# Kernel tuning notes

Hardware: AMD Instinct MI355X
Metric: run time of the kernel (lower is better)

Reference implementation:

```python
import jax, jax.numpy as jnp
import numpy as np

N = 8192            # n_nodes
E = 262144          # n_edges (avg degree 32)
IN_F, HID_F, OUT_F = 256, 128, 64


def _xavier(key, shape):
    fan_out, fan_in = shape
    lim = np.sqrt(6.0 / (fan_in + fan_out))
    return jax.random.uniform(key, shape, jnp.float32, -lim, lim)


def setup_inputs() -> dict:
    key = jax.random.key(0)
    k = jax.random.split(key, 7)
    edge_src = jnp.sort(jax.random.randint(k[0], (E,), 0, N))
    edge_dst = jax.random.randint(k[1], (E,), 0, N)
    h = jax.random.normal(k[2], (N, IN_F), jnp.float32)
    W0 = _xavier(k[3], (HID_F, IN_F))
    Wmu = _xavier(k[4], (OUT_F, HID_F))
    Wls = _xavier(k[5], (OUT_F, HID_F)) * 0.1  # keep exp(log_sigma) tame
    eps = jax.random.normal(k[6], (N, OUT_F), jnp.float32)
    return {"h": h, "W0": W0, "Wmu": Wmu, "Wls": Wls, "eps": eps,
            "edge_src": edge_src, "edge_dst": edge_dst}


def _gcn(edge_src, edge_dst, h, W, act=None):
    # a is the unweighted sparse adjacency given by (edge_src -> row, edge_dst -> col)
    n = h.shape[0]
    deg = jax.ops.segment_sum(jnp.ones(edge_src.shape[0], h.dtype), edge_src,
                              num_segments=n)                    # row-sum of a
    norm = jnp.clip(deg, 1.0, None) ** -0.5                      # d^{-1/2}, clamp(min=1)
    h = h * norm[:, None]                                        # pre-norm
    h = h @ W.T                                                  # Linear (no bias)
    h = jax.ops.segment_sum(h[edge_dst], edge_src, num_segments=n)  # a @ h (SpMM)
    h = h * norm[:, None]                                        # post-norm
    if act is not None:
        h = act(h)
    return h


def reference(h, W0, Wmu, Wls, eps, edge_src, edge_dst):
    h1 = _gcn(edge_src, edge_dst, h, W0, jax.nn.relu)            # gcn0 + ReLU
    mu = _gcn(edge_src, edge_dst, h1, Wmu)                       # gcn_mu
    log_sigma = _gcn(edge_src, edge_dst, h1, Wls)                # gcn_log_sigma
    z = mu + jnp.exp(log_sigma) * eps                            # q_z.rsample()
    logits = z @ z.T                                             # Bernoulli logits [N, N]
    return logits
```

## Files before the change

kernel.cpp:

```cpp
#include <hip/hip_runtime.h>
#include <hip/hip_bf16.h>
#include <cstdint>
#include <cstddef>

#define NN 8192
#define IN_F 256
#define HID_F 128
#define OUT_F 64

typedef __attribute__((ext_vector_type(8))) short short8v;
typedef __attribute__((ext_vector_type(4))) float f32x4;
typedef __attribute__((ext_vector_type(4))) unsigned short ushort4v;

static __device__ __forceinline__ unsigned short f2bf(float x) {
    unsigned int u = __float_as_uint(x);
    unsigned int r = (u + 0x7fffu + ((u >> 16) & 1u)) >> 16;
    return (unsigned short)r;
}
static __device__ __forceinline__ float bf2f(unsigned short u) {
    return __uint_as_float(((unsigned int)u) << 16);
}

__global__ void k_rowptr(const int* __restrict__ src, int* __restrict__ rp, int E, int N) {
    int i = blockIdx.x * blockDim.x + threadIdx.x;
    if (i >= E) return;
    int s = src[i];
    int p = (i == 0) ? -1 : src[i - 1];
    for (int n = p + 1; n <= s; ++n) rp[n] = i;
    if (i == E - 1) {
        for (int n = s + 1; n <= N; ++n) rp[n] = E;
    }
}

__global__ void k_norm(const int* __restrict__ rp, float* __restrict__ norm, int N) {
    int n = blockIdx.x * blockDim.x + threadIdx.x;
    if (n >= N) return;
    int d = rp[n + 1] - rp[n];
    float df = (float)(d < 1 ? 1 : d);
    norm[n] = rsqrtf(df);
}

__global__ void k_conv_h(const float* __restrict__ h, const float* __restrict__ norm,
                         unsigned short* __restrict__ hi, unsigned short* __restrict__ lo,
                         int total4) {
    int i = blockIdx.x * blockDim.x + threadIdx.x;
    if (i >= total4) return;
    int n = i / (IN_F / 4);
    float nv = norm[n];
    float4 v = reinterpret_cast<const float4*>(h)[i];
    ushort4v h4, l4;
    float x;
    x = v.x * nv; h4.x = f2bf(x); l4.x = f2bf(x - bf2f(h4.x));
    x = v.y * nv; h4.y = f2bf(x); l4.y = f2bf(x - bf2f(h4.y));
    x = v.z * nv; h4.z = f2bf(x); l4.z = f2bf(x - bf2f(h4.z));
    x = v.w * nv; h4.w = f2bf(x); l4.w = f2bf(x - bf2f(h4.w));
    reinterpret_cast<ushort4v*>(hi)[i] = h4;
    reinterpret_cast<ushort4v*>(lo)[i] = l4;
}

__global__ void k_conv_w(const float* __restrict__ W0, const float* __restrict__ Wmu,
                         const float* __restrict__ Wls,
                         unsigned short* __restrict__ W0h, unsigned short* __restrict__ W0l,
                         unsigned short* __restrict__ Wch, unsigned short* __restrict__ Wcl) {
    int i = blockIdx.x * blockDim.x + threadIdx.x;
    const int n0 = HID_F * IN_F;
    const int n1 = 2 * OUT_F * HID_F;
    if (i < n0) {
        float x = W0[i];
        unsigned short hh = f2bf(x);
        W0h[i] = hh; W0l[i] = f2bf(x - bf2f(hh));
    } else if (i < n0 + n1) {
        int j = i - n0;
        int r = j / HID_F, c = j % HID_F;
        float x = (r < OUT_F) ? Wmu[r * HID_F + c] : Wls[(r - OUT_F) * HID_F + c];
        unsigned short hh = f2bf(x);
        Wch[j] = hh; Wcl[j] = f2bf(x - bf2f(hh));
    }
}

template <int K, int MT, int NT>
__global__ __launch_bounds__(256) void k_gemm_bt(
    const unsigned short* __restrict__ Ahi, const unsigned short* __restrict__ Alo,
    const unsigned short* __restrict__ Bhi, const unsigned short* __restrict__ Blo,
    float* __restrict__ C, int ldc) {
    const int lane = threadIdx.x & 63;
    const int wid = threadIdx.x >> 6;
    const int wr = wid >> 1, wc = wid & 1;
    const long i0 = (long)blockIdx.x * (32 * MT) + wr * (16 * MT);
    const long j0 = (long)blockIdx.y * (32 * NT) + wc * (16 * NT);
    const int rl = lane & 15;
    const int kq = lane >> 4;

    f32x4 acc[MT][NT] = {};

    for (int kc = 0; kc < K; kc += 32) {
        const int kb = kc + kq * 8;
        short8v ah[MT], al[MT], bh[NT], bl[NT];
#pragma unroll
        for (int m = 0; m < MT; ++m) {
            size_t off = (size_t)(i0 + m * 16 + rl) * K + kb;
            ah[m] = *reinterpret_cast<const short8v*>(Ahi + off);
            al[m] = *reinterpret_cast<const short8v*>(Alo + off);
        }
#pragma unroll
        for (int n = 0; n < NT; ++n) {
            size_t off = (size_t)(j0 + n * 16 + rl) * K + kb;
            bh[n] = *reinterpret_cast<const short8v*>(Bhi + off);
            bl[n] = *reinterpret_cast<const short8v*>(Blo + off);
        }
#pragma unroll
        for (int m = 0; m < MT; ++m) {
#pragma unroll
            for (int n = 0; n < NT; ++n) {
                acc[m][n] = __builtin_amdgcn_mfma_f32_16x16x32_bf16(ah[m], bh[n], acc[m][n], 0, 0, 0);
                acc[m][n] = __builtin_amdgcn_mfma_f32_16x16x32_bf16(ah[m], bl[n], acc[m][n], 0, 0, 0);
                acc[m][n] = __builtin_amdgcn_mfma_f32_16x16x32_bf16(al[m], bh[n], acc[m][n], 0, 0, 0);
            }
        }
    }

    const int crow = (lane >> 4) * 4;
#pragma unroll
    for (int m = 0; m < MT; ++m) {
#pragma unroll
        for (int n = 0; n < NT; ++n) {
            size_t base = (size_t)(i0 + m * 16 + crow) * ldc + (size_t)(j0 + n * 16 + rl);
#pragma unroll
            for (int r = 0; r < 4; ++r)
                C[base + (size_t)r * ldc] = acc[m][n][r];
        }
    }
}

__global__ __launch_bounds__(128) void k_spmm1(
    const float* __restrict__ X, const int* __restrict__ rp, const int* __restrict__ dst,
    const float* __restrict__ norm, float* __restrict__ h1p) {
    int n = blockIdx.x;
    int t = threadIdx.x;
    int e0 = rp[n], e1 = rp[n + 1];
    float acc = 0.f;
    int e = e0;
    for (; e + 4 <= e1; e += 4) {
        int d0 = dst[e] * HID_F, d1 = dst[e + 1] * HID_F;
        int d2 = dst[e + 2] * HID_F, d3 = dst[e + 3] * HID_F;
        acc += X[d0 + t];
        acc += X[d1 + t];
        acc += X[d2 + t];
        acc += X[d3 + t];
    }
    for (; e < e1; ++e) acc += X[dst[e] * HID_F + t];
    float nv = norm[n];
    float v = acc * nv;
    v = v > 0.f ? v : 0.f;
    h1p[n * HID_F + t] = v * nv;
}

__global__ __launch_bounds__(128) void k_spmm2(
    const float* __restrict__ X, const int* __restrict__ rp, const int* __restrict__ dst,
    unsigned short* __restrict__ hi, unsigned short* __restrict__ lo) {
    int n = blockIdx.x;
    int t = threadIdx.x;
    int e0 = rp[n], e1 = rp[n + 1];
    float acc = 0.f;
    int e = e0;
    for (; e + 4 <= e1; e += 4) {
        int d0 = dst[e] * HID_F, d1 = dst[e + 1] * HID_F;
        int d2 = dst[e + 2] * HID_F, d3 = dst[e + 3] * HID_F;
        acc += X[d0 + t];
        acc += X[d1 + t];
        acc += X[d2 + t];
        acc += X[d3 + t];
    }
    for (; e < e1; ++e) acc += X[dst[e] * HID_F + t];
    unsigned short hh = f2bf(acc);
    hi[n * HID_F + t] = hh;
    lo[n * HID_F + t] = f2bf(acc - bf2f(hh));
}

__global__ void k_z(const float* __restrict__ P, const float* __restrict__ norm,
                    const float* __restrict__ eps,
                    unsigned short* __restrict__ zh, unsigned short* __restrict__ zl) {
    int i = blockIdx.x * blockDim.x + threadIdx.x;
    if (i >= NN * OUT_F) return;
    int n = i >> 6, f = i & 63;
    float nv = norm[n];
    float mu = P[n * HID_F + f] * nv;
    float ls = P[n * HID_F + 64 + f] * nv;
    float z = mu + expf(ls) * eps[i];
    unsigned short hh = f2bf(z);
    zh[i] = hh;
    zl[i] = f2bf(z - bf2f(hh));
}

extern "C" void kernel_launch(void* const* d_in, const int* in_sizes, int n_in,
                              void* d_out, int out_size, void* d_ws, size_t ws_size,
                              hipStream_t stream) {
    const float* h   = (const float*)d_in[0];
    const float* W0  = (const float*)d_in[1];
    const float* Wmu = (const float*)d_in[2];
    const float* Wls = (const float*)d_in[3];
    const float* eps = (const float*)d_in[4];
    const int* esrc  = (const int*)d_in[5];
    const int* edst  = (const int*)d_in[6];
    const int E = in_sizes[5];
    const int N = NN;

    char* w = (char*)d_ws;
    auto alloc = [&](size_t bytes) {
        char* p = w;
        w += (bytes + 511) & ~(size_t)511;
        return p;
    };
    int* rp             = (int*)alloc((N + 1) * sizeof(int));
    float* norm         = (float*)alloc(N * sizeof(float));
    unsigned short* Hh  = (unsigned short*)alloc((size_t)N * IN_F * 2);
    unsigned short* Hl  = (unsigned short*)alloc((size_t)N * IN_F * 2);
    unsigned short* W0h = (unsigned short*)alloc(HID_F * IN_F * 2);
    unsigned short* W0l = (unsigned short*)alloc(HID_F * IN_F * 2);
    unsigned short* Wch = (unsigned short*)alloc(2 * OUT_F * HID_F * 2);
    unsigned short* Wcl = (unsigned short*)alloc(2 * OUT_F * HID_F * 2);
    float* X1           = (float*)alloc((size_t)N * HID_F * sizeof(float));
    float* h1p          = (float*)alloc((size_t)N * HID_F * sizeof(float));
    unsigned short* Agh = (unsigned short*)alloc((size_t)N * HID_F * 2);
    unsigned short* Agl = (unsigned short*)alloc((size_t)N * HID_F * 2);
    float* P            = (float*)alloc((size_t)N * HID_F * sizeof(float));
    unsigned short* Zh  = (unsigned short*)alloc((size_t)N * OUT_F * 2);
    unsigned short* Zl  = (unsigned short*)alloc((size_t)N * OUT_F * 2);

    k_rowptr<<<(E + 255) / 256, 256, 0, stream>>>(esrc, rp, E, N);
    k_norm<<<(N + 255) / 256, 256, 0, stream>>>(rp, norm, N);
    k_conv_h<<<((N * IN_F / 4) + 255) / 256, 256, 0, stream>>>(h, norm, Hh, Hl, N * IN_F / 4);
    k_conv_w<<<(HID_F * IN_F + 2 * OUT_F * HID_F + 255) / 256, 256, 0, stream>>>(
        W0, Wmu, Wls, W0h, W0l, Wch, Wcl);

    k_gemm_bt<IN_F, 2, 2><<<dim3(N / 64, HID_F / 64), 256, 0, stream>>>(
        Hh, Hl, W0h, W0l, X1, HID_F);

    k_spmm1<<<N, 128, 0, stream>>>(X1, rp, edst, norm, h1p);
    k_spmm2<<<N, 128, 0, stream>>>(h1p, rp, edst, Agh, Agl);

    k_gemm_bt<HID_F, 2, 2><<<dim3(N / 64, HID_F / 64), 256, 0, stream>>>(
        Agh, Agl, Wch, Wcl, P, HID_F);

    k_z<<<((N * OUT_F) + 255) / 256, 256, 0, stream>>>(P, norm, eps, Zh, Zl);

    k_gemm_bt<OUT_F, 4, 4><<<dim3(N / 128, N / 128), 256, 0, stream>>>(
        Zh, Zl, Zh, Zl, (float*)d_out, N);
}
```

Before: 137.8 us.

## Fuse prep kernels, fold conversions into GEMMs, exploit symmetry of Z Z^T

Measured after the change: 153.1 us. +11.1%, slower.

```diff
diff --git a/kernel.cpp b/kernel.cpp
--- a/kernel.cpp
+++ b/kernel.cpp
@@ -4,6 +4,7 @@
 #include <cstddef>
 
 #define NN 8192
+#define EE 262144
 #define IN_F 256
 #define HID_F 128
 #define OUT_F 64
@@ -21,175 +22,316 @@
     return __uint_as_float(((unsigned int)u) << 16);
 }
 
-__global__ void k_rowptr(const int* __restrict__ src, int* __restrict__ rp, int E, int N) {
+static __device__ __forceinline__ void xpose4(f32x4& a, int lane) {
+    float a0 = a[0], a1 = a[1], a2 = a[2], a3 = a[3];
+    float s0 = __shfl_xor(a1, 1);
+    float s1 = __shfl_xor(a0, 1);
+    float s2 = __shfl_xor(a3, 1);
+    float s3 = __shfl_xor(a2, 1);
+    bool o1 = lane & 1;
+    float b0 = o1 ? s0 : a0;
+    float b1 = o1 ? a1 : s1;
+    float b2 = o1 ? s2 : a2;
+    float b3 = o1 ? a3 : s3;
+    float u0 = __shfl_xor(b2, 2);
+    float u1 = __shfl_xor(b3, 2);
+    float u2 = __shfl_xor(b0, 2);
+    float u3 = __shfl_xor(b1, 2);
+    bool o2 = lane & 2;
+    a[0] = o2 ? u0 : b0;
+    a[1] = o2 ? u1 : b1;
+    a[2] = o2 ? b2 : u2;
+    a[3] = o2 ? b3 : u3;
+}
+
+__global__ void k_prep(const int* __restrict__ src,
+                       const float* __restrict__ W0, const float* __restrict__ Wmu,
+                       const float* __restrict__ Wls,
+                       int* __restrict__ rp, float* __restrict__ norm,
+                       unsigned short* __restrict__ W0h, unsigned short* __restrict__ W0l,
+                       unsigned short* __restrict__ Wch, unsigned short* __restrict__ Wcl) {
     int i = blockIdx.x * blockDim.x + threadIdx.x;
-    if (i >= E) return;
-    int s = src[i];
-    int p = (i == 0) ? -1 : src[i - 1];
-    for (int n = p + 1; n <= s; ++n) rp[n] = i;
-    if (i == E - 1) {
-        for (int n = s + 1; n <= N; ++n) rp[n] = E;
-    }
-}
-
-__global__ void k_norm(const int* __restrict__ rp, float* __restrict__ norm, int N) {
-    int n = blockIdx.x * blockDim.x + threadIdx.x;
-    if (n >= N) return;
-    int d = rp[n + 1] - rp[n];
-    float df = (float)(d < 1 ? 1 : d);
-    norm[n] = rsqrtf(df);
-}
-
-__global__ void k_conv_h(const float* __restrict__ h, const float* __restrict__ norm,
-                         unsigned short* __restrict__ hi, unsigned short* __restrict__ lo,
-                         int total4) {
-    int i = blockIdx.x * blockDim.x + threadIdx.x;
-    if (i >= total4) return;
-    int n = i / (IN_F / 4);
-    float nv = norm[n];
-    float4 v = reinterpret_cast<const float4*>(h)[i];
-    ushort4v h4, l4;
-    float x;
-    x = v.x * nv; h4.x = f2bf(x); l4.x = f2bf(x - bf2f(h4.x));
-    x = v.y * nv; h4.y = f2bf(x); l4.y = f2bf(x - bf2f(h4.y));
-    x = v.z * nv; h4.z = f2bf(x); l4.z = f2bf(x - bf2f(h4.z));
-    x = v.w * nv; h4.w = f2bf(x); l4.w = f2bf(x - bf2f(h4.w));
-    reinterpret_cast<ushort4v*>(hi)[i] = h4;
-    reinterpret_cast<ushort4v*>(lo)[i] = l4;
-}
-
-__global__ void k_conv_w(const float* __restrict__ W0, const float* __restrict__ Wmu,
-                         const float* __restrict__ Wls,
-                         unsigned short* __restrict__ W0h, unsigned short* __restrict__ W0l,
-                         unsigned short* __restrict__ Wch, unsigned short* __restrict__ Wcl) {
-    int i = blockIdx.x * blockDim.x + threadIdx.x;
-    const int n0 = HID_F * IN_F;
-    const int n1 = 2 * OUT_F * HID_F;
-    if (i < n0) {
-        float x = W0[i];
-        unsigned short hh = f2bf(x);
-        W0h[i] = hh; W0l[i] = f2bf(x - bf2f(hh));
-    } else if (i < n0 + n1) {
-        int j = i - n0;
-        int r = j / HID_F, c = j % HID_F;
-        float x = (r < OUT_F) ? Wmu[r * HID_F + c] : Wls[(r - OUT_F) * HID_F + c];
-        unsigned short hh = f2bf(x);
-        Wch[j] = hh; Wcl[j] = f2bf(x - bf2f(hh));
-    }
-}
-
-template <int K, int MT, int NT>
-__global__ __launch_bounds__(256) void k_gemm_bt(
-    const unsigned short* __restrict__ Ahi, const unsigned short* __restrict__ Alo,
-    const unsigned short* __restrict__ Bhi, const unsigned short* __restrict__ Blo,
-    float* __restrict__ C, int ldc) {
-    const int lane = threadIdx.x & 63;
-    const int wid = threadIdx.x >> 6;
+    if (i <= NN) {
+        auto lb = [&](int key) {
+            int lo = 0, hi = EE;
+            while (lo < hi) { int mid = (lo + hi) >> 1; if (src[mid] < key) lo = mid + 1; else hi = mid; }
+            return lo;
+        };
+        int a = lb(i);
+        rp[i] = a;
+        if (i < NN) {
+            int d = lb(i + 1) - a;
+            norm[i] = rsqrtf((float)(d < 1 ? 1 : d));
+        }
+    } else {
+        int j = i - (NN + 1);
+        const int n0 = HID_F * IN_F;
+        const int n1 = 2 * OUT_F * HID_F;
+        if (j < n0) {
+            float x = W0[j];
+            unsigned short hh = f2bf(x);
+            W0h[j] = hh; W0l[j] = f2bf(x - bf2f(hh));
+        } else if (j < n0 + n1) {
+            int q = j - n0;
+            int r = q / HID_F, c = q % HID_F;
+            float x = (r < OUT_F) ? Wmu[r * HID_F + c] : Wls[(r - OUT_F) * HID_F + c];
+            unsigned short hh = f2bf(x);
+            Wch[q] = hh; Wcl[q] = f2bf(x - bf2f(hh));
+        }
+    }
+}
+
+__global__ __launch_bounds__(256) void k_gemm1(
+    const float* __restrict__ h, const float* __restrict__ norm,
+    const unsigned short* __restrict__ Bh16, const unsigned short* __restrict__ Bl16,
+    float* __restrict__ X1) {
+    const int lane = threadIdx.x & 63, wid = threadIdx.x >> 6;
     const int wr = wid >> 1, wc = wid & 1;
-    const long i0 = (long)blockIdx.x * (32 * MT) + wr * (16 * MT);
-    const long j0 = (long)blockIdx.y * (32 * NT) + wc * (16 * NT);
-    const int rl = lane & 15;
-    const int kq = lane >> 4;
-
-    f32x4 acc[MT][NT] = {};
-
-    for (int kc = 0; kc < K; kc += 32) {
+    const int i0 = blockIdx.x * 64 + wr * 32;
+    const int j0 = blockIdx.y * 64 + wc * 32;
+    const int rl = lane & 15, kq = lane >> 4;
+    f32x4 acc[2][2] = {};
+    float nv[2];
+    nv[0] = norm[i0 + rl];
+    nv[1] = norm[i0 + 16 + rl];
+    for (int kc = 0; kc < IN_F; kc += 32) {
         const int kb = kc + kq * 8;
-        short8v ah[MT], al[MT], bh[NT], bl[NT];
-#pragma unroll
-        for (int m = 0; m < MT; ++m) {
-            size_t off = (size_t)(i0 + m * 16 + rl) * K + kb;
-            ah[m] = *reinterpret_cast<const short8v*>(Ahi + off);
-            al[m] = *reinterpret_cast<const short8v*>(Alo + off);
-        }
-#pragma unroll
-        for (int n = 0; n < NT; ++n) {
-            size_t off = (size_t)(j0 + n * 16 + rl) * K + kb;
-            bh[n] = *reinterpret_cast<const short8v*>(Bhi + off);
-            bl[n] = *reinterpret_cast<const short8v*>(Blo + off);
-        }
-#pragma unroll
-        for (int m = 0; m < MT; ++m) {
-#pragma unroll
-            for (int n = 0; n < NT; ++n) {
+        short8v ah[2], al[2], bh[2], bl[2];
+#pragma unroll
+        for (int m = 0; m < 2; ++m) {
+            const float* p = h + (size_t)(i0 + m * 16 + rl) * IN_F + kb;
+            float4 v0 = *reinterpret_cast<const float4*>(p);
+            float4 v1 = *reinterpret_cast<const float4*>(p + 4);
+            float xs[8] = {v0.x, v0.y, v0.z, v0.w, v1.x, v1.y, v1.z, v1.w};
+#pragma unroll
+            for (int j = 0; j < 8; ++j) {
+                float x = xs[j] * nv[m];
+                unsigned short hh = f2bf(x);
+                ah[m][j] = (short)hh;
+                al[m][j] = (short)f2bf(x - bf2f(hh));
+            }
+        }
+#pragma unroll
+        for (int n = 0; n < 2; ++n) {
+            size_t off = (size_t)(j0 + n * 16 + rl) * IN_F + kb;
+            bh[n] = *reinterpret_cast<const short8v*>(Bh16 + off);
+            bl[n] = *reinterpret_cast<const short8v*>(Bl16 + off);
+        }
+#pragma unroll
+        for (int m = 0; m < 2; ++m)
+#pragma unroll
+            for (int n = 0; n < 2; ++n) {
                 acc[m][n] = __builtin_amdgcn_mfma_f32_16x16x32_bf16(ah[m], bh[n], acc[m][n], 0, 0, 0);
                 acc[m][n] = __builtin_amdgcn_mfma_f32_16x16x32_bf16(ah[m], bl[n], acc[m][n], 0, 0, 0);
                 acc[m][n] = __builtin_amdgcn_mfma_f32_16x16x32_bf16(al[m], bh[n], acc[m][n], 0, 0, 0);
             }
-        }
-    }
-
-    const int crow = (lane >> 4) * 4;
-#pragma unroll
-    for (int m = 0; m < MT; ++m) {
-#pragma unroll
-        for (int n = 0; n < NT; ++n) {
-            size_t base = (size_t)(i0 + m * 16 + crow) * ldc + (size_t)(j0 + n * 16 + rl);
-#pragma unroll
-            for (int r = 0; r < 4; ++r)
-                C[base + (size_t)r * ldc] = acc[m][n][r];
-        }
-    }
+    }
+    const int l2 = lane & 3, g4 = rl >> 2;
+#pragma unroll
+    for (int m = 0; m < 2; ++m)
+#pragma unroll
+        for (int n = 0; n < 2; ++n) {
+            xpose4(acc[m][n], lane);
+            *reinterpret_cast<f32x4*>(X1 + (size_t)(i0 + m * 16 + 4 * kq + l2) * HID_F +
+                                      j0 + n * 16 + 4 * g4) = acc[m][n];
+        }
 }
 
 __global__ __launch_bounds__(128) void k_spmm1(
     const float* __restrict__ X, const int* __restrict__ rp, const int* __restrict__ dst,
-    const float* __restrict__ norm, float* __restrict__ h1p) {
-    int n = blockIdx.x;
-    int t = threadIdx.x;
-    int e0 = rp[n], e1 = rp[n + 1];
-    float acc = 0.f;
-    int e = e0;
-    for (; e + 4 <= e1; e += 4) {
-        int d0 = dst[e] * HID_F, d1 = dst[e + 1] * HID_F;
-        int d2 = dst[e + 2] * HID_F, d3 = dst[e + 3] * HID_F;
-        acc += X[d0 + t];
-        acc += X[d1 + t];
-        acc += X[d2 + t];
-        acc += X[d3 + t];
-    }
-    for (; e < e1; ++e) acc += X[dst[e] * HID_F + t];
-    float nv = norm[n];
-    float v = acc * nv;
-    v = v > 0.f ? v : 0.f;
-    h1p[n * HID_F + t] = v * nv;
+    const float* __restrict__ norm, float* __restrict__ out) {
+    const int n = blockIdx.x;
+    const int t = threadIdx.x;
+    const int w = t >> 6, lane = t & 63;
+    const int sub = lane >> 5, c4 = lane & 31;
+    const int e0 = rp[n], e1 = rp[n + 1];
+    f32x4 acc = {0.f, 0.f, 0.f, 0.f};
+    int e = e0 + 2 * w + sub;
+    int dnext = (e < e1) ? dst[e] : 0;
+    while (e < e1) {
+        int d = dnext;
+        int en = e + 4;
+        dnext = (en < e1) ? dst[en] : 0;
+        f32x4 v = *reinterpret_cast<const f32x4*>(X + (size_t)d * HID_F + 4 * c4);
+        acc += v;
+        e = en;
+    }
+#pragma unroll
+    for (int q = 0; q < 4; ++q) acc[q] += __shfl_xor(acc[q], 32);
+    __shared__ f32x4 red[32];
+    if (w == 1 && sub == 0) red[c4] = acc;
+    __syncthreads();
+    if (w == 0 && sub == 0) {
+        f32x4 s = acc + red[c4];
+        float nv = norm[n];
+        f32x4 r;
+#pragma unroll
+        for (int q = 0; q < 4; ++q) {
+            float v = s[q] * nv;
+            v = v > 0.f ? v : 0.f;
+            r[q] = v * nv;
+        }
+        *reinterpret_cast<f32x4*>(out + (size_t)n * HID_F + 4 * c4) = r;
+    }
 }
 
 __global__ __launch_bounds__(128) void k_spmm2(
     const float* __restrict__ X, const int* __restrict__ rp, const int* __restrict__ dst,
-    unsigned short* __restrict__ hi, unsigned short* __restrict__ lo) {
-    int n = blockIdx.x;
-    int t = threadIdx.x;
-    int e0 = rp[n], e1 = rp[n + 1];
-    float acc = 0.f;
-    int e = e0;
-    for (; e + 4 <= e1; e += 4) {
-        int d0 = dst[e] * HID_F, d1 = dst[e + 1] * HID_F;
-        int d2 = dst[e + 2] * HID_F, d3 = dst[e + 3] * HID_F;
-        acc += X[d0 + t];
-        acc += X[d1 + t];
-        acc += X[d2 + t];
-        acc += X[d3 + t];
-    }
-    for (; e < e1; ++e) acc += X[dst[e] * HID_F + t];
-    unsigned short hh = f2bf(acc);
-    hi[n * HID_F + t] = hh;
-    lo[n * HID_F + t] = f2bf(acc - bf2f(hh));
-}
-
-__global__ void k_z(const float* __restrict__ P, const float* __restrict__ norm,
-                    const float* __restrict__ eps,
-                    unsigned short* __restrict__ zh, unsigned short* __restrict__ zl) {
-    int i = blockIdx.x * blockDim.x + threadIdx.x;
-    if (i >= NN * OUT_F) return;
-    int n = i >> 6, f = i & 63;
-    float nv = norm[n];
-    float mu = P[n * HID_F + f] * nv;
-    float ls = P[n * HID_F + 64 + f] * nv;
-    float z = mu + expf(ls) * eps[i];
-    unsigned short hh = f2bf(z);
-    zh[i] = hh;
-    zl[i] = f2bf(z - bf2f(hh));
+    unsigned short* __restrict__ Agh, unsigned short* __restrict__ Agl) {
+    const int n = blockIdx.x;
+    const int t = threadIdx.x;
+    const int w = t >> 6, lane = t & 63;
+    const int sub = lane >> 5, c4 = lane & 31;
+    const int e0 = rp[n], e1 = rp[n + 1];
+    f32x4 acc = {0.f, 0.f, 0.f, 0.f};
+    int e = e0 + 2 * w + sub;
+    int dnext = (e < e1) ? dst[e] : 0;
+    while (e < e1) {
+        int d = dnext;
+        int en = e + 4;
+        dnext = (en < e1) ? dst[en] : 0;
+        f32x4 v = *reinterpret_cast<const f32x4*>(X + (size_t)d * HID_F + 4 * c4);
+        acc += v;
+        e = en;
+    }
+#pragma unroll
+    for (int q = 0; q < 4; ++q) acc[q] += __shfl_xor(acc[q], 32);
+    __shared__ f32x4 red[32];
+    if (w == 1 && sub == 0) red[c4] = acc;
+    __syncthreads();
+    if (w == 0 && sub == 0) {
+        f32x4 s = acc + red[c4];
+        ushort4v sh, sl;
+#pragma unroll
+        for (int q = 0; q < 4; ++q) {
+            unsigned short hh = f2bf(s[q]);
+            sh[q] = hh;
+            sl[q] = f2bf(s[q] - bf2f(hh));
+        }
+        *reinterpret_cast<ushort4v*>(Agh + (size_t)n * HID_F + 4 * c4) = sh;
+        *reinterpret_cast<ushort4v*>(Agl + (size_t)n * HID_F + 4 * c4) = sl;
+    }
+}
+
+__global__ __launch_bounds__(256) void k_gemm2z(
+    const unsigned short* __restrict__ Ah16, const unsigned short* __restrict__ Al16,
+    const unsigned short* __restrict__ Bh16, const unsigned short* __restrict__ Bl16,
+    const float* __restrict__ norm, const float* __restrict__ eps,
+    unsigned short* __restrict__ Zh, unsigned short* __restrict__ Zl) {
+    const int lane = threadIdx.x & 63, wid = threadIdx.x >> 6;
+    const int wr = wid >> 1, wc = wid & 1;
+    const int R0 = blockIdx.x * 64;
+    const int rl = lane & 15, kq = lane >> 4;
+    f32x4 acc[2][4] = {};
+    for (int kc = 0; kc < HID_F; kc += 32) {
+        const int kb = kc + kq * 8;
+        short8v ah[2], al[2], bh[4], bl[4];
+#pragma unroll
+        for (int m = 0; m < 2; ++m) {
+            size_t off = (size_t)(R0 + wr * 32 + m * 16 + rl) * HID_F + kb;
+            ah[m] = *reinterpret_cast<const short8v*>(Ah16 + off);
+            al[m] = *reinterpret_cast<const short8v*>(Al16 + off);
+        }
+#pragma unroll
+        for (int n = 0; n < 4; ++n) {
+            size_t off = (size_t)(wc * 64 + n * 16 + rl) * HID_F + kb;
+            bh[n] = *reinterpret_cast<const short8v*>(Bh16 + off);
+            bl[n] = *reinterpret_cast<const short8v*>(Bl16 + off);
+        }
+#pragma unroll
+        for (int m = 0; m < 2; ++m)
+#pragma unroll
+            for (int n = 0; n < 4; ++n) {
+                acc[m][n] = __builtin_amdgcn_mfma_f32_16x16x32_bf16(ah[m], bh[n], acc[m][n], 0, 0, 0);
+                acc[m][n] = __builtin_amdgcn_mfma_f32_16x16x32_bf16(ah[m], bl[n], acc[m][n], 0, 0, 0);
+                acc[m][n] = __builtin_amdgcn_mfma_f32_16x16x32_bf16(al[m], bh[n], acc[m][n], 0, 0, 0);
+            }
+    }
+    __shared__ __align__(16) float Pl[64][132];
+#pragma unroll
+    for (int m = 0; m < 2; ++m)
+#pragma unroll
+        for (int n = 0; n < 4; ++n)
+#pragma unroll
+            for (int r = 0; r < 4; ++r)
+                Pl[wr * 32 + m * 16 + 4 * kq + r][wc * 64 + n * 16 + rl] = acc[m][n][r];
+    __syncthreads();
+    const int fg = threadIdx.x & 15;
+    const int rr = threadIdx.x >> 4;
+#pragma unroll
+    for (int p = 0; p < 4; ++p) {
+        int rloc = p * 16 + rr;
+        int row = R0 + rloc;
+        float nv = norm[row];
+        f32x4 mu = *reinterpret_cast<const f32x4*>(&Pl[rloc][4 * fg]);
+        f32x4 ls = *reinterpret_cast<const f32x4*>(&Pl[rloc][64 + 4 * fg]);
+        f32x4 ev = *reinterpret_cast<const f32x4*>(eps + (size_t)row * OUT_F + 4 * fg);
+        ushort4v zh, zl;
+#pragma unroll
+        for (int q = 0; q < 4; ++q) {
+            float z = mu[q] * nv + expf(ls[q] * nv) * ev[q];
+            unsigned short hh = f2bf(z);
+            zh[q] = hh;
+            zl[q] = f2bf(z - bf2f(hh));
+        }
+        *reinterpret_cast<ushort4v*>(Zh + (size_t)row * OUT_F + 4 * fg) = zh;
+        *reinterpret_cast<ushort4v*>(Zl + (size_t)row * OUT_F + 4 * fg) = zl;
+    }
+}
+
+__global__ __launch_bounds__(256) void k_gemm3(
+    const unsigned short* __restrict__ Zh, const unsigned short* __restrict__ Zl,
+    float* __restrict__ C) {
+    const int bi = blockIdx.x, bj = blockIdx.y;
+    if (bj < bi) return;
+    const int lane = threadIdx.x & 63, wid = threadIdx.x >> 6;
+    const int wr = wid >> 1, wc = wid & 1;
+    const int i0 = bi * 128 + wr * 64;
+    const int j0 = bj * 128 + wc * 64;
+    const int rl = lane & 15, kq = lane >> 4;
+    f32x4 acc[4][4] = {};
+    for (int kc = 0; kc < OUT_F; kc += 32) {
+        const int kb = kc + kq * 8;
+        short8v ah[4], al[4], bh[4], bl[4];
+#pragma unroll
+        for (int m = 0; m < 4; ++m) {
+            size_t off = (size_t)(i0 + m * 16 + rl) * OUT_F + kb;
+            ah[m] = *reinterpret_cast<const short8v*>(Zh + off);
+            al[m] = *reinterpret_cast<const short8v*>(Zl + off);
+        }
+#pragma unroll
+        for (int n = 0; n < 4; ++n) {
+            size_t off = (size_t)(j0 + n * 16 + rl) * OUT_F + kb;
+            bh[n] = *reinterpret_cast<const short8v*>(Zh + off);
+            bl[n] = *reinterpret_cast<const short8v*>(Zl + off);
+        }
+#pragma unroll
+        for (int m = 0; m < 4; ++m)
+#pragma unroll
+            for (int n = 0; n < 4; ++n) {
+                acc[m][n] = __builtin_amdgcn_mfma_f32_16x16x32_bf16(ah[m], bh[n], acc[m][n], 0, 0, 0);
+                acc[m][n] = __builtin_amdgcn_mfma_f32_16x16x32_bf16(ah[m], bl[n], acc[m][n], 0, 0, 0);
+                acc[m][n] = __builtin_amdgcn_mfma_f32_16x16x32_bf16(al[m], bh[n], acc[m][n], 0, 0, 0);
+            }
+    }
+    if (bj > bi) {
+#pragma unroll
+        for (int m = 0; m < 4; ++m)
+#pragma unroll
+            for (int n = 0; n < 4; ++n)
+#pragma unroll
+                for (int r = 0; r < 4; ++r)
+                    C[(size_t)(j0 + n * 16 + rl) * NN + (i0 + m * 16 + 4 * kq + r)] = acc[m][n][r];
+    }
+    const int l2 = lane & 3, g4 = rl >> 2;
+#pragma unroll
+    for (int m = 0; m < 4; ++m)
+#pragma unroll
+        for (int n = 0; n < 4; ++n) {
+            xpose4(acc[m][n], lane);
+            *reinterpret_cast<f32x4*>(C + (size_t)(i0 + m * 16 + 4 * kq + l2) * NN +
+                                      j0 + n * 16 + 4 * g4) = acc[m][n];
+        }
 }
 
 extern "C" void kernel_launch(void* const* d_in, const int* in_sizes, int n_in,
@@ -202,8 +344,6 @@
     const float* eps = (const float*)d_in[4];
     const int* esrc  = (const int*)d_in[5];
     const int* edst  = (const int*)d_in[6];
-    const int E = in_sizes[5];
-    const int N = NN;
 
     char* w = (char*)d_ws;
     auto alloc = [&](size_t bytes) {
@@ -211,39 +351,29 @@
         w += (bytes + 511) & ~(size_t)511;
         return p;
     };
-    int* rp             = (int*)alloc((N + 1) * sizeof(int));
-    float* norm         = (float*)alloc(N * sizeof(float));
-    unsigned short* Hh  = (unsigned short*)alloc((size_t)N * IN_F * 2);
-    unsigned short* Hl  = (unsigned short*)alloc((size_t)N * IN_F * 2);
+    int* rp             = (int*)alloc((NN + 1) * sizeof(int));
+    float* norm         = (float*)alloc(NN * sizeof(float));
     unsigned short* W0h = (unsigned short*)alloc(HID_F * IN_F * 2);
     unsigned short* W0l = (unsigned short*)alloc(HID_F * IN_F * 2);
     unsigned short* Wch = (unsigned short*)alloc(2 * OUT_F * HID_F * 2);
     unsigned short* Wcl = (unsigned short*)alloc(2 * OUT_F * HID_F * 2);
-    float* X1           = (float*)alloc((size_t)N * HID_F * sizeof(float));
-    float* h1p          = (float*)alloc((size_t)N * HID_F * sizeof(float));
-    unsigned short* Agh = (unsigned short*)alloc((size_t)N * HID_F * 2);
-    unsigned short* Agl = (unsigned short*)alloc((size_t)N * HID_F * 2);
-    float* P            = (float*)alloc((size_t)N * HID_F * sizeof(float));
-    unsigned short* Zh  = (unsigned short*)alloc((size_t)N * OUT_F * 2);
-    unsigned short* Zl  = (unsigned short*)alloc((size_t)N * OUT_F * 2);
-
-    k_rowptr<<<(E + 255) / 256, 256, 0, stream>>>(esrc, rp, E, N);
-    k_norm<<<(N + 255) / 256, 256, 0, stream>>>(rp, norm, N);
-    k_conv_h<<<((N * IN_F / 4) + 255) / 256, 256, 0, stream>>>(h, norm, Hh, Hl, N * IN_F / 4);
-    k_conv_w<<<(HID_F * IN_F + 2 * OUT_F * HID_F + 255) / 256, 256, 0, stream>>>(
-        W0, Wmu, Wls, W0h, W0l, Wch, Wcl);
-
-    k_gemm_bt<IN_F, 2, 2><<<dim3(N / 64, HID_F / 64), 256, 0, stream>>>(
-        Hh, Hl, W0h, W0l, X1, HID_F);
-
-    k_spmm1<<<N, 128, 0, stream>>>(X1, rp, edst, norm, h1p);
-    k_spmm2<<<N, 128, 0, stream>>>(h1p, rp, edst, Agh, Agl);
-
-    k_gemm_bt<HID_F, 2, 2><<<dim3(N / 64, HID_F / 64), 256, 0, stream>>>(
-        Agh, Agl, Wch, Wcl, P, HID_F);
-
-    k_z<<<((N * OUT_F) + 255) / 256, 256, 0, stream>>>(P, norm, eps, Zh, Zl);
-
-    k_gemm_bt<OUT_F, 4, 4><<<dim3(N / 128, N / 128), 256, 0, stream>>>(
-        Zh, Zl, Zh, Zl, (float*)d_out, N);
-}
+    float* X1           = (float*)alloc((size_t)NN * HID_F * sizeof(float));
+    float* h1p          = (float*)alloc((size_t)NN * HID_F * sizeof(float));
+    unsigned short* Agh = (unsigned short*)alloc((size_t)NN * HID_F * 2);
+    unsigned short* Agl = (unsigned short*)alloc((size_t)NN * HID_F * 2);
+    unsigned short* Zh  = (unsigned short*)alloc((size_t)NN * OUT_F * 2);
+    unsigned short* Zl  = (unsigned short*)alloc((size_t)NN * OUT_F * 2);
+
+    const int prep_threads = (NN + 1) + HID_F * IN_F + 2 * OUT_F * HID_F;
+    k_prep<<<(prep_threads + 255) / 256, 256, 0, stream>>>(
+        esrc, W0, Wmu, Wls, rp, norm, W0h, W0l, Wch, Wcl);
+
+    k_gemm1<<<dim3(NN / 64, HID_F / 64), 256, 0, stream>>>(h, norm, W0h, W0l, X1);
+
+    k_spmm1<<<NN, 128, 0, stream>>>(X1, rp, edst, norm, h1p);
+    k_spmm2<<<NN, 128, 0, stream>>>(h1p, rp, edst, Agh, Agl);
+
+    k_gemm2z<<<NN / 64, 256, 0, stream>>>(Agh, Agl, Wch, Wcl, norm, eps, Zh, Zl);
+
+    k_gemm3<<<dim3(NN / 128, NN / 128), 256, 0, stream>>>(Zh, Zl, (float*)d_out);
+}
```
